# Kernel optimization log

Hardware: AMD Instinct MI355X
Metric: run time of the kernel (lower is better)

## Reference

```python
import jax, jax.numpy as jnp
import numpy as np

PPU = 64          # points_per_unit
MARGIN = 0.1
INIT_LENGTHSCALE = 0.1


def setup_inputs() -> dict:
    key = jax.random.key(0)
    k1, k2, k3 = jax.random.split(key, 3)
    m, nc, nt, dim, dy = 8, 1024, 512, 2, 2
    xc = jax.random.uniform(k1, (m, nc, dim), jnp.float32)
    yc = jax.random.normal(k2, (m, nc, dy), jnp.float32)
    xt = jax.random.uniform(k3, (m, nt, dim), jnp.float32)
    # lengthscale_param = log(exp(init_ls) - 1) so softplus(param) == init_ls
    lengthscale_param = jnp.log(jnp.expm1(jnp.full((dim,), INIT_LENGTHSCALE, jnp.float32)))
    return {"xc": xc, "yc": yc, "xt": xt, "lengthscale_param": lengthscale_param}


def reference(xc, yc, xt, lengthscale_param):
    m, _, dim = xc.shape
    lengthscale = 1e-5 + jax.nn.softplus(lengthscale_param)  # (dim,)

    # append density channel of ones
    yc1 = jnp.concatenate([yc, jnp.ones(yc.shape[:-1] + (1,), yc.dtype)], axis=-1)

    # adaptive grid over concat(xc, xt)
    x_all = jnp.concatenate([xc, xt], axis=-2)
    xmin = x_all.min(axis=-2)  # (m, dim)
    xmax = x_all.max(axis=-2)  # (m, dim)
    Nf = jnp.ceil((0.5 * (xmax - xmin) + MARGIN) * PPU).max(axis=0)
    Nf = 2.0 ** jnp.ceil(jnp.log2(Nf))
    N = np.asarray(Nf).astype(np.int64)  # concrete per-dim half-widths (grid size)

    axes = [jnp.arange(-int(n), int(n) + 1, dtype=xc.dtype) for n in N]  # inclusive, like torch.range
    base = jnp.stack(jnp.meshgrid(*axes, indexing='ij'), axis=-1)  # (n1,...,ndim, dim)
    x_mid = 0.5 * (xmin + xmax)  # (m, dim)
    x_grid = x_mid.reshape((m,) + (1,) * dim + (dim,)) + base[None] / PPU  # (m, n1,...,ndim, dim)
    x_grid_flat = x_grid.reshape(m, -1, dim)  # (m, ng, dim)

    # RBF weights: exp(-0.5 * ||(g - c)/ls||^2) via expanded quadratic form
    a = x_grid_flat / lengthscale  # (m, ng, dim)
    b = xc / lengthscale           # (m, nc, dim)
    dist2 = ((a * a).sum(-1)[:, :, None]
             + (b * b).sum(-1)[:, None, :]
             - 2.0 * jnp.einsum('bgd,bcd->bgc', a, b))
    weights = jnp.exp(-0.5 * jnp.maximum(dist2, 0.0))  # (m, ng, nc)

    z_flat = weights @ yc1  # (m, ng, dy+1)
    z_grid = z_flat.reshape(x_grid.shape[:-1] + (yc1.shape[-1],))
    return (x_grid, z_grid)
```

## Files before the change

### kernel.cpp

```cpp
#include <hip/hip_runtime.h>
#include <math.h>

#define M_BATCH 8
#define NC 1024
#define NTGT 512
#define G_DIM 129
#define NG (G_DIM * G_DIM)
#define N_OUT (G_DIM * 3)
#define TM 32
#define TN 32
#define KCH 128
#define NKCH (NC / KCH)
#define LDA 136
#define MT_TILES 5
#define NT_TILES 13

typedef __attribute__((ext_vector_type(8))) _Float16 half8;
typedef __attribute__((ext_vector_type(2))) _Float16 half2v;
typedef __attribute__((ext_vector_type(4))) float floatx4;

#if defined(__has_builtin)
#if __has_builtin(__builtin_amdgcn_exp2f)
#define FAST_EXP2(x) __builtin_amdgcn_exp2f(x)
#endif
#endif
#ifndef FAST_EXP2
#define FAST_EXP2(x) exp2f(x)
#endif

__global__ __launch_bounds__(256) void fused_kernel(
        const float* __restrict__ xc, const float* __restrict__ yc,
        const float* __restrict__ xt, const float* __restrict__ lsp,
        float* __restrict__ out_grid, float* __restrict__ out_z) {
    const int tid = threadIdx.x;
    const int nt = blockIdx.x;
    const int mt = blockIdx.y;
    const int m  = blockIdx.z;

    __shared__ _Float16 As[TM * LDA];
    __shared__ _Float16 Bs[TN * LDA];
    __shared__ float4 sm[256];

    float mn0 = 1e30f, mx0 = -1e30f, mn1 = 1e30f, mx1 = -1e30f;
    const float2* pc = (const float2*)(xc + m * NC * 2);
    for (int i = tid; i < NC; i += 256) {
        float2 p = pc[i];
        mn0 = fminf(mn0, p.x); mx0 = fmaxf(mx0, p.x);
        mn1 = fminf(mn1, p.y); mx1 = fmaxf(mx1, p.y);
    }
    const float2* pt = (const float2*)(xt + m * NTGT * 2);
    for (int i = tid; i < NTGT; i += 256) {
        float2 p = pt[i];
        mn0 = fminf(mn0, p.x); mx0 = fmaxf(mx0, p.x);
        mn1 = fminf(mn1, p.y); mx1 = fmaxf(mx1, p.y);
    }
    sm[tid] = make_float4(mn0, mx0, mn1, mx1);
    __syncthreads();
    for (int s = 128; s > 0; s >>= 1) {
        if (tid < s) {
            float4 a = sm[tid], b = sm[tid + s];
            sm[tid] = make_float4(fminf(a.x, b.x), fmaxf(a.y, b.y),
                                  fminf(a.z, b.z), fmaxf(a.w, b.w));
        }
        __syncthreads();
    }
    const float mid0 = 0.5f * (sm[0].x + sm[0].y);
    const float mid1 = 0.5f * (sm[0].z + sm[0].w);

    const float Kc = 0.84932180028801904272f;
    const float ls0 = 1e-5f + log1pf(expf(lsp[0]));
    const float ls1 = 1e-5f + log1pf(expf(lsp[1]));
    const float s0 = Kc / ls0, s1 = Kc / ls1;
    const float inv_ppu = 1.0f / 64.0f;

    if (nt == 0) {
        const int nrows = min(TM, G_DIM - mt * TM);
        float2* og = (float2*)out_grid + (size_t)m * NG;
        for (int g = tid; g < nrows * G_DIM; g += 256) {
            const int r = g / G_DIM;
            const int iyy = g - r * G_DIM;
            const int ixg = mt * TM + r;
            og[(size_t)ixg * G_DIM + iyy] =
                make_float2(mid0 + (float)(ixg - 64) * inv_ppu,
                            mid1 + (float)(iyy - 64) * inv_ppu);
        }
    }

    const int h = tid >> 6;
    const int c2 = (tid & 63) * 2;
    const float gstep = inv_ppu * s0;
    const float gxs_base = (mid0 + (float)(mt * TM + h * 8 - 64) * inv_ppu) * s0;
    const int ng0 = nt * TN + h * 8;
    const int iy0 = ng0 / 3;
    const int ch0 = ng0 - 3 * iy0;

    const float4* xcm4 = (const float4*)(xc + m * NC * 2);
    const float4* ycm4 = (const float4*)(yc + m * NC * 2);

    const int wm = h >> 1;
    const int wn = h & 1;
    const int lane = tid & 63;
    const int ln = lane & 15;
    const int q = lane >> 4;

    floatx4 acc = {0.f, 0.f, 0.f, 0.f};

    for (int kc = 0; kc < NKCH; ++kc) {
        const int cpb = (kc * KCH + c2) >> 1;
        const float4 xq = xcm4[cpb];
        const float4 yq = ycm4[cpb];
        const float cx0 = xq.x * s0, cy0 = xq.y * s1;
        const float cx1 = xq.z * s0, cy1 = xq.w * s1;

        float gxs = gxs_base;
#pragma unroll
        for (int i = 0; i < 8; ++i) {
            const float d0 = gxs - cx0;
            const float d1 = gxs - cx1;
            const float w0 = FAST_EXP2(-(d0 * d0));
            const float w1 = FAST_EXP2(-(d1 * d1));
            *(half2v*)&As[(h * 8 + i) * LDA + c2] =
                (half2v){(_Float16)w0, (_Float16)w1};
            gxs += gstep;
        }

        int iyr = iy0, chr = ch0;
#pragma unroll
        for (int i = 0; i < 8; ++i) {
            const float gys = (mid1 + (float)(iyr - 64) * inv_ppu) * s1;
            const float d0 = gys - cy0;
            const float d1 = gys - cy1;
            const float wy0 = FAST_EXP2(-(d0 * d0));
            const float wy1 = FAST_EXP2(-(d1 * d1));
            const float ya = (chr == 0) ? yq.x : (chr == 1) ? yq.y : 1.0f;
            const float yb = (chr == 0) ? yq.z : (chr == 1) ? yq.w : 1.0f;
            *(half2v*)&Bs[(h * 8 + i) * LDA + c2] =
                (half2v){(_Float16)(wy0 * ya), (_Float16)(wy1 * yb)};
            if (++chr == 3) { chr = 0; ++iyr; }
        }
        __syncthreads();

#pragma unroll
        for (int kk = 0; kk < 4; ++kk) {
            half8 a = *(const half8*)&As[(wm * 16 + ln) * LDA + kk * 32 + q * 8];
            half8 b = *(const half8*)&Bs[(wn * 16 + ln) * LDA + kk * 32 + q * 8];
            acc = __builtin_amdgcn_mfma_f32_16x16x32_f16(a, b, acc, 0, 0, 0);
        }
        __syncthreads();
    }

    const int ngl = nt * TN + wn * 16 + ln;
    if (ngl < N_OUT) {
        float* oz = out_z + (size_t)m * NG * 3;
        const int ixb = mt * TM + wm * 16 + q * 4;
#pragma unroll
        for (int rr = 0; rr < 4; ++rr) {
            const int ixg = ixb + rr;
            if (ixg < G_DIM) oz[(size_t)ixg * N_OUT + ngl] = acc[rr];
        }
    }
}

extern "C" void kernel_launch(void* const* d_in, const int* in_sizes, int n_in,
                              void* d_out, int out_size, void* d_ws, size_t ws_size,
                              hipStream_t stream) {
    const float* xc  = (const float*)d_in[0];
    const float* yc  = (const float*)d_in[1];
    const float* xt  = (const float*)d_in[2];
    const float* lsp = (const float*)d_in[3];

    float* out_grid = (float*)d_out;
    float* out_z = out_grid + (size_t)M_BATCH * NG * 2;

    dim3 grid(NT_TILES, MT_TILES, M_BATCH);
    fused_kernel<<<grid, 256, 0, stream>>>(xc, yc, xt, lsp, out_grid, out_z);
}
```

Baseline: 74.06 us.

## Generate MFMA operands in registers with 16x16 tiles and split-K across waves

```diff
diff --git a/kernel.cpp b/kernel.cpp
--- a/kernel.cpp
+++ b/kernel.cpp
@@ -7,16 +7,12 @@
 #define G_DIM 129
 #define NG (G_DIM * G_DIM)
 #define N_OUT (G_DIM * 3)
-#define TM 32
-#define TN 32
-#define KCH 128
-#define NKCH (NC / KCH)
-#define LDA 136
-#define MT_TILES 5
-#define NT_TILES 13
+#define MT_TILES 9
+#define NT_TILES 25
+#define SPLIT 4
+#define KSP (NC / SPLIT)
 
 typedef __attribute__((ext_vector_type(8))) _Float16 half8;
-typedef __attribute__((ext_vector_type(2))) _Float16 half2v;
 typedef __attribute__((ext_vector_type(4))) float floatx4;
 
 #if defined(__has_builtin)
@@ -28,18 +24,18 @@
 #define FAST_EXP2(x) exp2f(x)
 #endif
 
-__global__ __launch_bounds__(256) void fused_kernel(
+__global__ __launch_bounds__(256, 7) void fused_kernel(
         const float* __restrict__ xc, const float* __restrict__ yc,
         const float* __restrict__ xt, const float* __restrict__ lsp,
         float* __restrict__ out_grid, float* __restrict__ out_z) {
     const int tid = threadIdx.x;
-    const int nt = blockIdx.x;
-    const int mt = blockIdx.y;
-    const int m  = blockIdx.z;
+    const int t = blockIdx.x;
+    const int m = blockIdx.y;
+    const int mt = t / NT_TILES;
+    const int nt = t - mt * NT_TILES;
 
-    __shared__ _Float16 As[TM * LDA];
-    __shared__ _Float16 Bs[TN * LDA];
     __shared__ float4 sm[256];
+    __shared__ floatx4 cs[SPLIT][64];
 
     float mn0 = 1e30f, mx0 = -1e30f, mn1 = 1e30f, mx1 = -1e30f;
     const float2* pc = (const float2*)(xc + m * NC * 2);
@@ -74,91 +70,80 @@
     const float inv_ppu = 1.0f / 64.0f;
 
     if (nt == 0) {
-        const int nrows = min(TM, G_DIM - mt * TM);
+        const int r0 = mt * 16;
+        const int nrows = min(16, G_DIM - r0);
         float2* og = (float2*)out_grid + (size_t)m * NG;
         for (int g = tid; g < nrows * G_DIM; g += 256) {
             const int r = g / G_DIM;
             const int iyy = g - r * G_DIM;
-            const int ixg = mt * TM + r;
+            const int ixg = r0 + r;
             og[(size_t)ixg * G_DIM + iyy] =
                 make_float2(mid0 + (float)(ixg - 64) * inv_ppu,
                             mid1 + (float)(iyy - 64) * inv_ppu);
         }
     }
 
-    const int h = tid >> 6;
-    const int c2 = (tid & 63) * 2;
-    const float gstep = inv_ppu * s0;
-    const float gxs_base = (mid0 + (float)(mt * TM + h * 8 - 64) * inv_ppu) * s0;
-    const int ng0 = nt * TN + h * 8;
-    const int iy0 = ng0 / 3;
-    const int ch0 = ng0 - 3 * iy0;
-
-    const float4* xcm4 = (const float4*)(xc + m * NC * 2);
-    const float4* ycm4 = (const float4*)(yc + m * NC * 2);
-
-    const int wm = h >> 1;
-    const int wn = h & 1;
+    const int w = tid >> 6;
     const int lane = tid & 63;
     const int ln = lane & 15;
     const int q = lane >> 4;
 
+    const int ixg = mt * 16 + ln;
+    const int ng0 = nt * 16 + ln;
+    const int iy = ng0 / 3;
+    const int ch = ng0 - 3 * iy;
+
+    const float gxs = (mid0 + (float)(ixg - 64) * inv_ppu) * s0;
+    const float gys = (mid1 + (float)(iy - 64) * inv_ppu) * s1;
+
+    const float4* xc4 = (const float4*)(xc + m * NC * 2);
+    const float4* yc4 = (const float4*)(yc + m * NC * 2);
+
     floatx4 acc = {0.f, 0.f, 0.f, 0.f};
+    const int pbase = w * (KSP / 2) + q * 4;
 
-    for (int kc = 0; kc < NKCH; ++kc) {
-        const int cpb = (kc * KCH + c2) >> 1;
-        const float4 xq = xcm4[cpb];
-        const float4 yq = ycm4[cpb];
-        const float cx0 = xq.x * s0, cy0 = xq.y * s1;
-        const float cx1 = xq.z * s0, cy1 = xq.w * s1;
-
-        float gxs = gxs_base;
+    for (int kk = 0; kk < KSP / 32; ++kk) {
+        const int p = pbase + kk * 16;
+        half8 a, b;
 #pragma unroll
-        for (int i = 0; i < 8; ++i) {
-            const float d0 = gxs - cx0;
-            const float d1 = gxs - cx1;
-            const float w0 = FAST_EXP2(-(d0 * d0));
-            const float w1 = FAST_EXP2(-(d1 * d1));
-            *(half2v*)&As[(h * 8 + i) * LDA + c2] =
-                (half2v){(_Float16)w0, (_Float16)w1};
-            gxs += gstep;
+        for (int h = 0; h < 2; ++h) {
+            const float4 x0 = xc4[p + 2 * h + 0];
+            const float4 x1 = xc4[p + 2 * h + 1];
+            const float4 y0 = yc4[p + 2 * h + 0];
+            const float4 y1 = yc4[p + 2 * h + 1];
+            const float cxs[4] = {x0.x, x0.z, x1.x, x1.z};
+            const float cys[4] = {x0.y, x0.w, x1.y, x1.w};
+            const float ye[4]  = {y0.x, y0.z, y1.x, y1.z};
+            const float yo[4]  = {y0.y, y0.w, y1.y, y1.w};
+#pragma unroll
+            for (int j = 0; j < 4; ++j) {
+                const float dx = fmaf(-cxs[j], s0, gxs);
+                a[4 * h + j] = (_Float16)FAST_EXP2(-(dx * dx));
+                const float dy = fmaf(-cys[j], s1, gys);
+                const float wy = FAST_EXP2(-(dy * dy));
+                const float yv = (ch == 0) ? ye[j] : (ch == 1) ? yo[j] : 1.0f;
+                b[4 * h + j] = (_Float16)(wy * yv);
+            }
         }
-
-        int iyr = iy0, chr = ch0;
-#pragma unroll
-        for (int i = 0; i < 8; ++i) {
-            const float gys = (mid1 + (float)(iyr - 64) * inv_ppu) * s1;
-            const float d0 = gys - cy0;
-            const float d1 = gys - cy1;
-            const float wy0 = FAST_EXP2(-(d0 * d0));
-            const float wy1 = FAST_EXP2(-(d1 * d1));
-            const float ya = (chr == 0) ? yq.x : (chr == 1) ? yq.y : 1.0f;
-            const float yb = (chr == 0) ? yq.z : (chr == 1) ? yq.w : 1.0f;
-            *(half2v*)&Bs[(h * 8 + i) * LDA + c2] =
-                (half2v){(_Float16)(wy0 * ya), (_Float16)(wy1 * yb)};
-            if (++chr == 3) { chr = 0; ++iyr; }
-        }
-        __syncthreads();
-
-#pragma unroll
-        for (int kk = 0; kk < 4; ++kk) {
-            half8 a = *(const half8*)&As[(wm * 16 + ln) * LDA + kk * 32 + q * 8];
-            half8 b = *(const half8*)&Bs[(wn * 16 + ln) * LDA + kk * 32 + q * 8];
-            acc = __builtin_amdgcn_mfma_f32_16x16x32_f16(a, b, acc, 0, 0, 0);
-        }
-        __syncthreads();
+        acc = __builtin_amdgcn_mfma_f32_16x16x32_f16(a, b, acc, 0, 0, 0);
     }
 
-    const int ngl = nt * TN + wn * 16 + ln;
-    if (ngl < N_OUT) {
-        float* oz = out_z + (size_t)m * NG * 3;
-        const int ixb = mt * TM + wm * 16 + q * 4;
-#pragma unroll
-        for (int rr = 0; rr < 4; ++rr) {
-            const int ixg = ixb + rr;
-            if (ixg < G_DIM) oz[(size_t)ixg * N_OUT + ngl] = acc[rr];
-        }
-    }
+    cs[w][lane] = acc;
+    __syncthreads();
+
+    const int cl = tid & 15;
+    const int r = tid >> 4;
+    const int lsrc = (r >> 2) * 16 + cl;
+    const int rr = r & 3;
+    float v = ((const float*)&cs[0][lsrc])[rr]
+            + ((const float*)&cs[1][lsrc])[rr]
+            + ((const float*)&cs[2][lsrc])[rr]
+            + ((const float*)&cs[3][lsrc])[rr];
+
+    const int ixo = mt * 16 + r;
+    const int ngo = nt * 16 + cl;
+    if (ixo < G_DIM && ngo < N_OUT)
+        out_z[(size_t)m * NG * 3 + (size_t)ixo * N_OUT + ngo] = v;
 }
 
 extern "C" void kernel_launch(void* const* d_in, const int* in_sizes, int n_in,
@@ -172,6 +157,6 @@
     float* out_grid = (float*)d_out;
     float* out_z = out_grid + (size_t)M_BATCH * NG * 2;
 
-    dim3 grid(NT_TILES, MT_TILES, M_BATCH);
+    dim3 grid(MT_TILES * NT_TILES, M_BATCH);
     fused_kernel<<<grid, 256, 0, stream>>>(xc, yc, xt, lsp, out_grid, out_z);
 }
```

Result: slower. 83.75 us (+13.1%).

## Double-buffer LDS weight tiles and split K across two wave groups with 512 threads

Applied to the files above, without the earlier changes.

```diff
diff --git a/kernel.cpp b/kernel.cpp
--- a/kernel.cpp
+++ b/kernel.cpp
@@ -14,6 +14,7 @@
 #define LDA 136
 #define MT_TILES 5
 #define NT_TILES 13
+#define ABYTES (TM * LDA * 2)
 
 typedef __attribute__((ext_vector_type(8))) _Float16 half8;
 typedef __attribute__((ext_vector_type(2))) _Float16 half2v;
@@ -28,44 +29,50 @@
 #define FAST_EXP2(x) exp2f(x)
 #endif
 
-__global__ __launch_bounds__(256) void fused_kernel(
+__global__ __launch_bounds__(512) void fused_kernel(
         const float* __restrict__ xc, const float* __restrict__ yc,
         const float* __restrict__ xt, const float* __restrict__ lsp,
         float* __restrict__ out_grid, float* __restrict__ out_z) {
     const int tid = threadIdx.x;
-    const int nt = blockIdx.x;
-    const int mt = blockIdx.y;
-    const int m  = blockIdx.z;
+    const int t = blockIdx.x;
+    const int m = blockIdx.y;
+    const int mt = t / NT_TILES;
+    const int nt = t - mt * NT_TILES;
 
-    __shared__ _Float16 As[TM * LDA];
-    __shared__ _Float16 Bs[TN * LDA];
-    __shared__ float4 sm[256];
+    __shared__ __align__(16) char lds_raw[4 * ABYTES];
 
-    float mn0 = 1e30f, mx0 = -1e30f, mn1 = 1e30f, mx1 = -1e30f;
-    const float2* pc = (const float2*)(xc + m * NC * 2);
-    for (int i = tid; i < NC; i += 256) {
-        float2 p = pc[i];
-        mn0 = fminf(mn0, p.x); mx0 = fmaxf(mx0, p.x);
-        mn1 = fminf(mn1, p.y); mx1 = fmaxf(mx1, p.y);
+    {
+        float mn0 = 1e30f, mx0 = -1e30f, mn1 = 1e30f, mx1 = -1e30f;
+        const float2* pc = (const float2*)(xc + m * NC * 2);
+        for (int i = tid; i < NC; i += 512) {
+            float2 p = pc[i];
+            mn0 = fminf(mn0, p.x); mx0 = fmaxf(mx0, p.x);
+            mn1 = fminf(mn1, p.y); mx1 = fmaxf(mx1, p.y);
+        }
+        const float2* pt = (const float2*)(xt + m * NTGT * 2);
+        {
+            float2 p = pt[tid];
+            mn0 = fminf(mn0, p.x); mx0 = fmaxf(mx0, p.x);
+            mn1 = fminf(mn1, p.y); mx1 = fmaxf(mx1, p.y);
+        }
+        float4* sm = (float4*)lds_raw;
+        sm[tid] = make_float4(mn0, mx0, mn1, mx1);
     }
-    const float2* pt = (const float2*)(xt + m * NTGT * 2);
-    for (int i = tid; i < NTGT; i += 256) {
-        float2 p = pt[i];
-        mn0 = fminf(mn0, p.x); mx0 = fmaxf(mx0, p.x);
-        mn1 = fminf(mn1, p.y); mx1 = fmaxf(mx1, p.y);
+    __syncthreads();
+    {
+        float4* sm = (float4*)lds_raw;
+        for (int s = 256; s > 0; s >>= 1) {
+            if (tid < s) {
+                float4 a = sm[tid], b = sm[tid + s];
+                sm[tid] = make_float4(fminf(a.x, b.x), fmaxf(a.y, b.y),
+                                      fminf(a.z, b.z), fmaxf(a.w, b.w));
+            }
+            __syncthreads();
+        }
     }
-    sm[tid] = make_float4(mn0, mx0, mn1, mx1);
+    const float mid0 = 0.5f * (((float4*)lds_raw)[0].x + ((float4*)lds_raw)[0].y);
+    const float mid1 = 0.5f * (((float4*)lds_raw)[0].z + ((float4*)lds_raw)[0].w);
     __syncthreads();
-    for (int s = 128; s > 0; s >>= 1) {
-        if (tid < s) {
-            float4 a = sm[tid], b = sm[tid + s];
-            sm[tid] = make_float4(fminf(a.x, b.x), fmaxf(a.y, b.y),
-                                  fminf(a.z, b.z), fmaxf(a.w, b.w));
-        }
-        __syncthreads();
-    }
-    const float mid0 = 0.5f * (sm[0].x + sm[0].y);
-    const float mid1 = 0.5f * (sm[0].z + sm[0].w);
 
     const float Kc = 0.84932180028801904272f;
     const float ls0 = 1e-5f + log1pf(expf(lsp[0]));
@@ -74,89 +81,100 @@
     const float inv_ppu = 1.0f / 64.0f;
 
     if (nt == 0) {
-        const int nrows = min(TM, G_DIM - mt * TM);
+        const int r0 = mt * TM;
+        const int nrows = min(TM, G_DIM - r0);
         float2* og = (float2*)out_grid + (size_t)m * NG;
-        for (int g = tid; g < nrows * G_DIM; g += 256) {
+        for (int g = tid; g < nrows * G_DIM; g += 512) {
             const int r = g / G_DIM;
             const int iyy = g - r * G_DIM;
-            const int ixg = mt * TM + r;
+            const int ixg = r0 + r;
             og[(size_t)ixg * G_DIM + iyy] =
                 make_float2(mid0 + (float)(ixg - 64) * inv_ppu,
                             mid1 + (float)(iyy - 64) * inv_ppu);
         }
     }
 
-    const int h = tid >> 6;
     const int c2 = (tid & 63) * 2;
+    const int r0s = tid >> 6;
+    const float4* xc4 = (const float4*)(xc + m * NC * 2);
+    const float4* yc4 = (const float4*)(yc + m * NC * 2);
+    const float gxs_base = (mid0 + (float)(mt * TM - 64) * inv_ppu) * s0;
     const float gstep = inv_ppu * s0;
-    const float gxs_base = (mid0 + (float)(mt * TM + h * 8 - 64) * inv_ppu) * s0;
-    const int ng0 = nt * TN + h * 8;
-    const int iy0 = ng0 / 3;
-    const int ch0 = ng0 - 3 * iy0;
 
-    const float4* xcm4 = (const float4*)(xc + m * NC * 2);
-    const float4* ycm4 = (const float4*)(yc + m * NC * 2);
-
-    const int wm = h >> 1;
-    const int wn = h & 1;
+    const int w = tid >> 6;
+    const int g = w >> 2;
+    const int wm = (w >> 1) & 1;
+    const int wn = w & 1;
     const int lane = tid & 63;
     const int ln = lane & 15;
     const int q = lane >> 4;
 
     floatx4 acc = {0.f, 0.f, 0.f, 0.f};
 
+    auto stage = [&](int kc, int buf) {
+        const int cp = (kc * KCH >> 1) + (tid & 63);
+        const float4 xq = xc4[cp];
+        const float4 yq = yc4[cp];
+        const float cx0 = xq.x * s0, cx1 = xq.z * s0;
+        const float cy0 = xq.y * s1, cy1 = xq.w * s1;
+        _Float16* Ab = (_Float16*)(lds_raw + (size_t)buf * 2 * ABYTES);
+        _Float16* Bb = (_Float16*)(lds_raw + (size_t)buf * 2 * ABYTES + ABYTES);
+#pragma unroll
+        for (int i = 0; i < 4; ++i) {
+            const int r = r0s + 8 * i;
+            const float gxs = gxs_base + (float)r * gstep;
+            const float dx0 = gxs - cx0;
+            const float dx1 = gxs - cx1;
+            *(half2v*)&Ab[r * LDA + c2] =
+                (half2v){(_Float16)FAST_EXP2(-(dx0 * dx0)),
+                         (_Float16)FAST_EXP2(-(dx1 * dx1))};
+            const int n = nt * TN + r;
+            const int iy = (int)(((unsigned)n * 0xAAABu) >> 17);
+            const int ch = n - 3 * iy;
+            const float gys = (mid1 + (float)(iy - 64) * inv_ppu) * s1;
+            const float dy0 = gys - cy0;
+            const float dy1 = gys - cy1;
+            const float wy0 = FAST_EXP2(-(dy0 * dy0));
+            const float wy1 = FAST_EXP2(-(dy1 * dy1));
+            const float ya = (ch == 0) ? yq.x : (ch == 1) ? yq.y : 1.0f;
+            const float yb = (ch == 0) ? yq.z : (ch == 1) ? yq.w : 1.0f;
+            *(half2v*)&Bb[r * LDA + c2] =
+                (half2v){(_Float16)(wy0 * ya), (_Float16)(wy1 * yb)};
+        }
+    };
+
+    stage(0, 0);
+    __syncthreads();
+
     for (int kc = 0; kc < NKCH; ++kc) {
-        const int cpb = (kc * KCH + c2) >> 1;
-        const float4 xq = xcm4[cpb];
-        const float4 yq = ycm4[cpb];
-        const float cx0 = xq.x * s0, cy0 = xq.y * s1;
-        const float cx1 = xq.z * s0, cy1 = xq.w * s1;
-
-        float gxs = gxs_base;
+        const int buf = kc & 1;
+        const _Float16* Ab = (const _Float16*)(lds_raw + (size_t)buf * 2 * ABYTES);
+        const _Float16* Bb = (const _Float16*)(lds_raw + (size_t)buf * 2 * ABYTES + ABYTES);
 #pragma unroll
-        for (int i = 0; i < 8; ++i) {
-            const float d0 = gxs - cx0;
-            const float d1 = gxs - cx1;
-            const float w0 = FAST_EXP2(-(d0 * d0));
-            const float w1 = FAST_EXP2(-(d1 * d1));
-            *(half2v*)&As[(h * 8 + i) * LDA + c2] =
-                (half2v){(_Float16)w0, (_Float16)w1};
-            gxs += gstep;
-        }
-
-        int iyr = iy0, chr = ch0;
-#pragma unroll
-        for (int i = 0; i < 8; ++i) {
-            const float gys = (mid1 + (float)(iyr - 64) * inv_ppu) * s1;
-            const float d0 = gys - cy0;
-            const float d1 = gys - cy1;
-            const float wy0 = FAST_EXP2(-(d0 * d0));
-            const float wy1 = FAST_EXP2(-(d1 * d1));
-            const float ya = (chr == 0) ? yq.x : (chr == 1) ? yq.y : 1.0f;
-            const float yb = (chr == 0) ? yq.z : (chr == 1) ? yq.w : 1.0f;
-            *(half2v*)&Bs[(h * 8 + i) * LDA + c2] =
-                (half2v){(_Float16)(wy0 * ya), (_Float16)(wy1 * yb)};
-            if (++chr == 3) { chr = 0; ++iyr; }
-        }
-        __syncthreads();
-
-#pragma unroll
-        for (int kk = 0; kk < 4; ++kk) {
-            half8 a = *(const half8*)&As[(wm * 16 + ln) * LDA + kk * 32 + q * 8];
-            half8 b = *(const half8*)&Bs[(wn * 16 + ln) * LDA + kk * 32 + q * 8];
+        for (int kk = 0; kk < 2; ++kk) {
+            half8 a = *(const half8*)&Ab[(wm * 16 + ln) * LDA + g * 64 + kk * 32 + q * 8];
+            half8 b = *(const half8*)&Bb[(wn * 16 + ln) * LDA + g * 64 + kk * 32 + q * 8];
             acc = __builtin_amdgcn_mfma_f32_16x16x32_f16(a, b, acc, 0, 0, 0);
         }
+        if (kc + 1 < NKCH) stage(kc + 1, buf ^ 1);
         __syncthreads();
     }
 
-    const int ngl = nt * TN + wn * 16 + ln;
-    if (ngl < N_OUT) {
-        float* oz = out_z + (size_t)m * NG * 3;
-        const int ixb = mt * TM + wm * 16 + q * 4;
+    floatx4* cs = (floatx4*)lds_raw;
+    if (g == 1) cs[(size_t)(w & 3) * 64 + lane] = acc;
+    __syncthreads();
+    if (g == 0) {
+        const floatx4 o = cs[(size_t)w * 64 + lane];
+        const int ngo = nt * TN + wn * 16 + ln;
+        if (ngo < N_OUT) {
+            float* oz = out_z + (size_t)m * NG * 3;
+            const int ixb = mt * TM + wm * 16 + q * 4;
 #pragma unroll
-        for (int rr = 0; rr < 4; ++rr) {
-            const int ixg = ixb + rr;
-            if (ixg < G_DIM) oz[(size_t)ixg * N_OUT + ngl] = acc[rr];
+            for (int rr = 0; rr < 4; ++rr) {
+                const int ixg = ixb + rr;
+                if (ixg < G_DIM)
+                    oz[(size_t)ixg * N_OUT + ngo] = acc[rr] + o[rr];
+            }
         }
     }
 }
@@ -172,6 +190,6 @@
     float* out_grid = (float*)d_out;
     float* out_z = out_grid + (size_t)M_BATCH * NG * 2;
 
-    dim3 grid(NT_TILES, MT_TILES, M_BATCH);
-    fused_kernel<<<grid, 256, 0, stream>>>(xc, yc, xt, lsp, out_grid, out_z);
+    dim3 grid(MT_TILES * NT_TILES, M_BATCH);
+    fused_kernel<<<grid, 512, 0, stream>>>(xc, yc, xt, lsp, out_grid, out_z);
 }
```

Measured after the change: 73.24 us. Within noise of the previous version (-1.1%).
